# Optimization experiments

Measured on AMD Instinct MI355X. Metric: run time of the kernel, lower is better.

The kernel has to match this reference:

```python
import jax, jax.numpy as jnp
import numpy as np
import math


def _alibi_slopes(h):
    # h must be a power of 2 here (h=16); matches pow2slopes in the source
    start = 2.0 ** (-2.0 ** (-(math.log2(h) - 3.0)))
    return jnp.asarray([start ** (i + 1) for i in range(h)], dtype=jnp.float32)


def setup_inputs() -> dict:
    key = jax.random.key(0)
    ks = jax.random.split(key, 7)
    B, N, d, h, r = 2, 2048, 1024, 16, 32
    dk = d // h
    x = jax.random.normal(ks[0], (B, N, d), dtype=jnp.float32)
    # causal additive mask (standard usage of the optional `mask` arg)
    i = jnp.arange(N)[:, None]
    j = jnp.arange(N)[None, :]
    mask = jnp.where(j > i, jnp.float32(-1e9), jnp.float32(0.0))[None, None]  # [1,1,N,N]
    s = 1.0 / math.sqrt(d)
    Wq = jax.random.normal(ks[1], (d, d), dtype=jnp.float32) * s
    Wk = jax.random.normal(ks[2], (d, d), dtype=jnp.float32) * s
    Wv = jax.random.normal(ks[3], (d, d), dtype=jnp.float32) * s
    # orthogonal init of U, as in nn.init.orthogonal_
    U, _ = jnp.linalg.qr(jax.random.normal(ks[4], (dk, r), dtype=jnp.float32))
    Wproj = jax.random.normal(ks[5], (d, h * r), dtype=jnp.float32) * (1.0 / math.sqrt(h * r))
    return {"x": x, "mask": mask, "Wq": Wq, "Wk": Wk, "Wv": Wv, "U": U,
            "Wproj": Wproj, "rel_bias_tokens": N}


def reference(x, mask, Wq, Wk, Wv, U, Wproj, rel_bias_tokens):
    B, N, d = x.shape
    dk, r = U.shape
    h = d // dk

    def lowrank_proj(W):
        # Linear(d,d,bias=False) then per-head low-rank projection by U
        y = (x @ W.T).reshape(B, N, h, dk)          # [B,N,h,dk]
        return jnp.einsum('bnhk,kr->bhnr', y, U)     # [B,h,N,r]

    q = lowrank_proj(Wq)
    k = lowrank_proj(Wk)
    v = lowrank_proj(Wv)

    # scores scaled by sqrt(dk) (NOT sqrt(r)) -- faithful to source
    att = jnp.einsum('bhnr,bhmr->bhnm', q, k) / math.sqrt(dk)  # [B,h,N,N]

    # q_len == k_len branch: alibi bias + mask
    i = jnp.arange(rel_bias_tokens)[:, None]
    j = jnp.arange(rel_bias_tokens)[None, :]
    dist = jnp.maximum(j - i, 0).astype(att.dtype)             # clamp_min(0)
    slopes = _alibi_slopes(h)
    att = att + (-slopes[:, None, None] * dist)[None] + mask

    z = jnp.einsum('bhnm,bhmr->bhnr', jax.nn.softmax(att, axis=-1), v)
    z = z.transpose(0, 2, 1, 3).reshape(B, N, h * r)
    # dropout is identity in eval
    return z @ Wproj.T
```

## Files before the change

kernel.cpp:

```cpp
#include <hip/hip_runtime.h>
#include <hip/hip_bf16.h>
#include <stdint.h>

typedef unsigned short u16;
typedef __attribute__((ext_vector_type(4))) short short4v;
typedef __attribute__((ext_vector_type(8))) short short8;
typedef __attribute__((ext_vector_type(4))) float f32x4;

#define NB 2
#define NN 2048
#define ND 1024
#define NH 16
#define NR 32
#define NM (NB*NN)
#define NHR 512
#define NQKV 1536

static __device__ __forceinline__ u16 f2bf(float f) {
  union { float f; uint32_t u; } v; v.f = f;
  uint32_t r = v.u + 0x7fffu + ((v.u >> 16) & 1u);
  return (u16)(r >> 16);
}
static __device__ __forceinline__ u16 fastbf(float f) {
  union { float f; uint32_t u; } v; v.f = f;
  return (u16)((v.u + 0x8000u) >> 16);
}

typedef __attribute__((address_space(1))) unsigned int as1_u32;
typedef __attribute__((address_space(3))) unsigned int as3_u32;

static __device__ __forceinline__ void async_copy16(void* lds, const void* g) {
  __builtin_amdgcn_global_load_lds((as1_u32*)(uintptr_t)g,
                                   (as3_u32*)(uint32_t)(uintptr_t)lds,
                                   16, 0, 0);
}

#define SB_BARRIER() do {                                        \
    asm volatile("s_waitcnt vmcnt(0) lgkmcnt(0)" ::: "memory");  \
    __syncthreads();                                             \
  } while (0)

__global__ __launch_bounds__(256, 2)
void prep(const float* __restrict__ x, const float* __restrict__ Wproj,
          const float* __restrict__ Wq, const float* __restrict__ Wk,
          const float* __restrict__ Wv, const float* __restrict__ U,
          u16* __restrict__ xb, u16* __restrict__ Wpb, u16* __restrict__ WcT) {
  __shared__ float sU[64 * 32];
  const int blk = blockIdx.x;
  const int tid = threadIdx.x;
  if (blk < 2304) {
    const float* in = (blk < 2048) ? x : Wproj;
    u16* o = (blk < 2048) ? xb : Wpb;
    const int i = ((blk < 2048) ? blk : (blk - 2048)) * 256 + tid;
    const float4* p = (const float4*)in + (size_t)i * 2;
    float4 a = p[0], b2 = p[1];
    short8 v;
    v[0] = f2bf(a.x);  v[1] = f2bf(a.y);  v[2] = f2bf(a.z);  v[3] = f2bf(a.w);
    v[4] = f2bf(b2.x); v[5] = f2bf(b2.y); v[6] = f2bf(b2.z); v[7] = f2bf(b2.w);
    *((short8*)o + i) = v;
  } else {
    #pragma unroll
    for (int t = 0; t < 2; ++t)
      ((float4*)sU)[t * 256 + tid] = ((const float4*)U)[t * 256 + tid];
    __syncthreads();
    const int local = blk - 2304;
    const int wh = local >> 2;
    const int w = wh >> 4, head = wh & 15;
    const float* W = (w == 0) ? Wq : (w == 1 ? Wk : Wv);
    const int i = (local & 3) * 256 + tid;
    const float* Wcol = W + (size_t)head * 64 * ND + i;
    float acc[32];
    #pragma unroll
    for (int rr = 0; rr < 32; ++rr) acc[rr] = 0.f;
    for (int kk = 0; kk < 64; ++kk) {
      const float wv = Wcol[(size_t)kk * ND];
      const float4* u4 = (const float4*)&sU[kk * 32];
      #pragma unroll
      for (int r4 = 0; r4 < 8; ++r4) {
        float4 u = u4[r4];
        acc[r4 * 4 + 0] += wv * u.x;
        acc[r4 * 4 + 1] += wv * u.y;
        acc[r4 * 4 + 2] += wv * u.z;
        acc[r4 * 4 + 3] += wv * u.w;
      }
    }
    const float sc = (w == 0) ? 0.125f : 1.0f;
    const int colBase = w * 512 + head * 32;
    #pragma unroll
    for (int rr = 0; rr < 32; ++rr)
      WcT[(size_t)(colBase + rr) * ND + i] = f2bf(acc[rr] * sc);
  }
}

template<int EPI>
__global__ __launch_bounds__(256, 3)
void gemm_bt(const u16* __restrict__ A, int lda,
             const u16* __restrict__ BT, int ldb, int K,
             u16* __restrict__ o0, u16* __restrict__ o1, u16* __restrict__ o2,
             float* __restrict__ fo) {
  __shared__ __align__(16) u16 lA[2][64 * 64];
  __shared__ __align__(16) u16 lB[2][128 * 64];
  const int tid = threadIdx.x;
  const int lane = tid & 63, quad = lane >> 4, l16 = lane & 15;
  const int wave = tid >> 6;
  const int wn = wave * 32;
  const int GX = gridDim.x;
  const int flat = blockIdx.y * GX + blockIdx.x;
  const int xcd = flat & 7, s = flat >> 3;
  const int per = gridDim.y >> 3;
  const int brow = xcd * per + s / GX, bcol = s % GX;
  const int rowBase = brow * 64, colBase = bcol * 128;

  f32x4 acc[4][2];
  #pragma unroll
  for (int i = 0; i < 4; ++i)
    #pragma unroll
    for (int j = 0; j < 2; ++j)
      acc[i][j] = (f32x4){0.f, 0.f, 0.f, 0.f};

  #define GSTAGE(t_, bf_) do {                                              \
    const int kt0 = (t_) * 64;                                              \
    _Pragma("unroll")                                                       \
    for (int it = 0; it < 6; ++it) {                                        \
      const int cid = it * 256 + tid;                                       \
      if (it < 2) {                                                         \
        const int row = cid >> 3, pc = cid & 7;                             \
        const int gc = pc ^ (row & 7);                                      \
        async_copy16(&lA[bf_][cid * 8],                                     \
                     &A[(size_t)(rowBase + row) * lda + kt0 + gc * 8]);     \
      } else {                                                              \
        const int c2 = cid - 512;                                           \
        const int row = c2 >> 3, pc = c2 & 7;                               \
        const int gc = pc ^ (row & 7);                                      \
        async_copy16(&lB[bf_][c2 * 8],                                      \
                     &BT[(size_t)(colBase + row) * ldb + kt0 + gc * 8]);    \
      }                                                                     \
    }                                                                       \
  } while (0)

  const int NT = K / 64;
  GSTAGE(0, 0);
  int buf = 0;
  for (int t = 0; t < NT; ++t) {
    SB_BARRIER();
    if (t + 1 < NT) GSTAGE(t + 1, buf ^ 1);
    #pragma unroll
    for (int ks = 0; ks < 64; ks += 32) {
      short8 fa[4], fb[2];
      #pragma unroll
      for (int t2 = 0; t2 < 4; ++t2) {
        const int ra = t2 * 16 + l16;
        const int pa = ((ks >> 3) + quad) ^ (ra & 7);
        fa[t2] = *(const short8*)&lA[buf][ra * 64 + pa * 8];
      }
      #pragma unroll
      for (int t2 = 0; t2 < 2; ++t2) {
        const int rb = wn + t2 * 16 + l16;
        const int pb = ((ks >> 3) + quad) ^ (rb & 7);
        fb[t2] = *(const short8*)&lB[buf][rb * 64 + pb * 8];
      }
      #pragma unroll
      for (int mt = 0; mt < 4; ++mt)
        #pragma unroll
        for (int nt = 0; nt < 2; ++nt)
          acc[mt][nt] = __builtin_amdgcn_mfma_f32_16x16x32_bf16(
              fa[mt], fb[nt], acc[mt][nt], 0, 0, 0);
    }
    buf ^= 1;
  }
  #undef GSTAGE

  #pragma unroll
  for (int mt = 0; mt < 4; ++mt) {
    const int gr0 = rowBase + mt * 16 + quad * 4;
    #pragma unroll
    for (int nt = 0; nt < 2; ++nt) {
      const int c = colBase + wn + nt * 16 + l16;
      #pragma unroll
      for (int j = 0; j < 4; ++j) {
        const float v = acc[mt][nt][j];
        const int row = gr0 + j;
        if (EPI == 0) {
          fo[(size_t)row * 1024 + c] = v;
        } else {
          const int b = row >> 11, n = row & (NN - 1);
          const int w = c >> 9, ch = c & 511, head = ch >> 5, rr = ch & 31;
          if (w == 0)
            o0[(size_t)(((b * NH + head) * NN + n)) * NR + rr] = f2bf(v);
          else if (w == 1)
            o1[(size_t)(((b * NH + head) * NN + n)) * NR + rr] = f2bf(v);
          else
            o2[(size_t)((b * NH + head) * NR + rr) * NN + n] = f2bf(v);
        }
      }
    }
  }
}

__global__ __launch_bounds__(256, 6)
void flash_attn(const u16* __restrict__ q, const u16* __restrict__ k,
                const u16* __restrict__ vt, u16* __restrict__ z) {
  __shared__ __align__(16) u16 lK[2][64 * 32];
  __shared__ __align__(16) u16 lV[2][32 * 64];
  const int bh = blockIdx.x;
  const int b = bh >> 4, head = bh & 15;
  const int tid = threadIdx.x;
  const int lane = tid & 63, quad = lane >> 4, l16 = lane & 15;
  const int wave = tid >> 6;
  const int qblk = gridDim.y - 1 - blockIdx.y;
  const int qb0 = qblk * 64;
  const int qbase = qb0 + wave * 16;
  const int qq = qbase + l16;

  const u16* qp = q  + (size_t)bh * NN * NR;
  const u16* kp = k  + (size_t)bh * NN * NR;
  const u16* vp = vt + (size_t)bh * NR * NN;

  const short8 bq = *(const short8*)&qp[(size_t)(qbase + l16) * NR + quad * 8];

  f32x4 Ot0 = (f32x4){0.f,0.f,0.f,0.f};
  f32x4 Ot1 = (f32x4){0.f,0.f,0.f,0.f};
  float ls = 0.f;

  const int krow = tid >> 2, kc = tid & 3;
  const int vrow = tid >> 3, vpc = tid & 7;
  const int vgc = vpc ^ (vrow & 7);

  #define STAGE(kt_, buf_) do {                                            \
    const int m0_ = (kt_) * 64;                                            \
    async_copy16(&lK[buf_][tid * 8], &kp[(size_t)(m0_ + krow) * NR + kc * 8]); \
    async_copy16(&lV[buf_][tid * 8], &vp[(size_t)vrow * NN + m0_ + vgc * 8]);  \
  } while (0)

  STAGE(0, 0);
  int buf = 0;
  for (int kt = 0; kt <= qblk; ++kt) {
    SB_BARRIER();
    if (kt < qblk) STAGE(kt + 1, buf ^ 1);

    const int m0 = kt * 64;
    f32x4 s[4];
    const f32x4 zero = (f32x4){0.f,0.f,0.f,0.f};
    #pragma unroll
    for (int g = 0; g < 4; ++g) {
      const short8 ak = *(const short8*)&lK[buf][(16 * g + l16) * 32 + quad * 8];
      s[g] = __builtin_amdgcn_mfma_f32_16x16x32_bf16(ak, bq, zero, 0, 0, 0);
    }
    if (kt == qblk) {
      #pragma unroll
      for (int g = 0; g < 4; ++g)
        #pragma unroll
        for (int j = 0; j < 4; ++j)
          if (m0 + 16 * g + quad * 4 + j > qq) s[g][j] = -1e30f;
    }
    #pragma unroll
    for (int g = 0; g < 4; ++g) {
      const float p0 = __expf(s[g][0]), p1 = __expf(s[g][1]);
      const float p2 = __expf(s[g][2]), p3 = __expf(s[g][3]);
      ls += (p0 + p1) + (p2 + p3);
      short4v bp;
      bp[0] = fastbf(p0); bp[1] = fastbf(p1); bp[2] = fastbf(p2); bp[3] = fastbf(p3);
      const int c0 = 2 * g + (quad >> 1), off = (quad & 1) * 4;
      const short4v av0 = *(const short4v*)
          &lV[buf][l16 * 64 + ((c0 ^ (l16 & 7)) * 8) + off];
      const short4v av1 = *(const short4v*)
          &lV[buf][(16 + l16) * 64 + ((c0 ^ ((16 + l16) & 7)) * 8) + off];
      Ot0 = __builtin_amdgcn_mfma_f32_16x16x16bf16_1k(av0, bp, Ot0, 0, 0, 0);
      Ot1 = __builtin_amdgcn_mfma_f32_16x16x16bf16_1k(av1, bp, Ot1, 0, 0, 0);
    }
    buf ^= 1;
  }
  #undef STAGE

  ls += __shfl_xor(ls, 16);
  ls += __shfl_xor(ls, 32);
  const float inv = 1.f / ls;

  short4v o0, o1;
  #pragma unroll
  for (int j = 0; j < 4; ++j) {
    o0[j] = f2bf(Ot0[j] * inv);
    o1[j] = f2bf(Ot1[j] * inv);
  }
  u16* zr = z + (size_t)(b * NN + qq) * NHR + head * NR;
  *(short4v*)&zr[quad * 4]      = o0;
  *(short4v*)&zr[16 + quad * 4] = o1;
}

extern "C" void kernel_launch(void* const* d_in, const int* in_sizes, int n_in,
                              void* d_out, int out_size, void* d_ws, size_t ws_size,
                              hipStream_t stream) {
  const float* x     = (const float*)d_in[0];
  const float* Wq    = (const float*)d_in[2];
  const float* Wk    = (const float*)d_in[3];
  const float* Wv    = (const float*)d_in[4];
  const float* U     = (const float*)d_in[5];
  const float* Wproj = (const float*)d_in[6];
  float* out = (float*)d_out;

  u16* ws  = (u16*)d_ws;
  u16* xb  = ws;
  u16* z   = ws;
  u16* Wpb = ws + (size_t)4 * 1024 * 1024;
  u16* WcT = Wpb + (size_t)512 * 1024;
  u16* q   = ws + (size_t)6 * 1024 * 1024;
  u16* kk  = q  + (size_t)NB * NH * NN * NR;
  u16* vt  = kk + (size_t)NB * NH * NN * NR;

  prep<<<2496, 256, 0, stream>>>(x, Wproj, Wq, Wk, Wv, U, xb, Wpb, WcT);
  gemm_bt<1><<<dim3(NQKV / 128, NM / 64), 256, 0, stream>>>(
      xb, ND, WcT, ND, ND, q, kk, vt, nullptr);
  flash_attn<<<dim3(NB * NH, NN / 64), 256, 0, stream>>>(q, kk, vt, z);
  gemm_bt<0><<<dim3(ND / 128, NM / 64), 256, 0, stream>>>(
      z, NHR, Wpb, NHR, NHR, nullptr, nullptr, nullptr, out);
}
```

Before: 160.4 us.

## Process 128 query rows per attention block, reuse K/V tiles, use exp2

The flash attention kernel now handles 128 query rows per block, with each wave owning two 16-row fragments. Each staged K/V tile therefore feeds twice as many MFMAs, halving K/V staging and barriers per query. The grid pairs long and short causal blocks by interleaving qblk order, and the log2e factor is folded into the Q weight scale so the kernel can use the native exp2. The costs are higher register pressure, occupancy lowered to 2 in launch bounds, and half as many blocks in flight.

Result: slower. 165.5 us (+3.2%).

```diff
diff --git a/kernel.cpp b/kernel.cpp
--- a/kernel.cpp
+++ b/kernel.cpp
@@ -25,6 +25,12 @@
   union { float f; uint32_t u; } v; v.f = f;
   return (u16)((v.u + 0x8000u) >> 16);
 }
+
+#if __has_builtin(__builtin_amdgcn_exp2f)
+#define EXP2(x) __builtin_amdgcn_exp2f(x)
+#else
+#define EXP2(x) exp2f(x)
+#endif
 
 typedef __attribute__((address_space(1))) unsigned int as1_u32;
 typedef __attribute__((address_space(3))) unsigned int as3_u32;
@@ -84,7 +90,7 @@
         acc[r4 * 4 + 3] += wv * u.w;
       }
     }
-    const float sc = (w == 0) ? 0.125f : 1.0f;
+    const float sc = (w == 0) ? 0.125f * 1.44269504088896340736f : 1.0f;
     const int colBase = w * 512 + head * 32;
     #pragma unroll
     for (int rr = 0; rr < 32; ++rr)
@@ -197,7 +203,7 @@
   }
 }
 
-__global__ __launch_bounds__(256, 6)
+__global__ __launch_bounds__(256, 2)
 void flash_attn(const u16* __restrict__ q, const u16* __restrict__ k,
                 const u16* __restrict__ vt, u16* __restrict__ z) {
   __shared__ __align__(16) u16 lK[2][64 * 32];
@@ -207,20 +213,26 @@
   const int tid = threadIdx.x;
   const int lane = tid & 63, quad = lane >> 4, l16 = lane & 15;
   const int wave = tid >> 6;
-  const int qblk = gridDim.y - 1 - blockIdx.y;
-  const int qb0 = qblk * 64;
-  const int qbase = qb0 + wave * 16;
-  const int qq = qbase + l16;
+  const int y = blockIdx.y;
+  const int half = gridDim.y >> 1;
+  const int qblk = (y < half) ? (gridDim.y - 1 - y) : (y - half);
+  const int qb0 = qblk * 128;
+  const int qbase = qb0 + wave * 32;
 
   const u16* qp = q  + (size_t)bh * NN * NR;
   const u16* kp = k  + (size_t)bh * NN * NR;
   const u16* vp = vt + (size_t)bh * NR * NN;
 
-  const short8 bq = *(const short8*)&qp[(size_t)(qbase + l16) * NR + quad * 8];
-
-  f32x4 Ot0 = (f32x4){0.f,0.f,0.f,0.f};
-  f32x4 Ot1 = (f32x4){0.f,0.f,0.f,0.f};
-  float ls = 0.f;
+  const short8 bq0 = *(const short8*)&qp[(size_t)(qbase + l16) * NR + quad * 8];
+  const short8 bq1 = *(const short8*)&qp[(size_t)(qbase + 16 + l16) * NR + quad * 8];
+
+  f32x4 Ot[2][2];
+  #pragma unroll
+  for (int qf = 0; qf < 2; ++qf)
+    #pragma unroll
+    for (int hh = 0; hh < 2; ++hh)
+      Ot[qf][hh] = (f32x4){0.f, 0.f, 0.f, 0.f};
+  float lsum[2] = {0.f, 0.f};
 
   const int krow = tid >> 2, kc = tid & 3;
   const int vrow = tid >> 3, vpc = tid & 7;
@@ -234,57 +246,71 @@
 
   STAGE(0, 0);
   int buf = 0;
-  for (int kt = 0; kt <= qblk; ++kt) {
+  const int NT = 2 * qblk + 2;
+  for (int kt = 0; kt < NT; ++kt) {
     SB_BARRIER();
-    if (kt < qblk) STAGE(kt + 1, buf ^ 1);
+    if (kt + 1 < NT) STAGE(kt + 1, buf ^ 1);
 
     const int m0 = kt * 64;
-    f32x4 s[4];
-    const f32x4 zero = (f32x4){0.f,0.f,0.f,0.f};
+    f32x4 s[2][4];
+    const f32x4 zero = (f32x4){0.f, 0.f, 0.f, 0.f};
     #pragma unroll
     for (int g = 0; g < 4; ++g) {
       const short8 ak = *(const short8*)&lK[buf][(16 * g + l16) * 32 + quad * 8];
-      s[g] = __builtin_amdgcn_mfma_f32_16x16x32_bf16(ak, bq, zero, 0, 0, 0);
-    }
-    if (kt == qblk) {
-      #pragma unroll
-      for (int g = 0; g < 4; ++g)
+      s[0][g] = __builtin_amdgcn_mfma_f32_16x16x32_bf16(ak, bq0, zero, 0, 0, 0);
+      s[1][g] = __builtin_amdgcn_mfma_f32_16x16x32_bf16(ak, bq1, zero, 0, 0, 0);
+    }
+    #pragma unroll
+    for (int qf = 0; qf < 2; ++qf) {
+      const int qrow0 = qbase + qf * 16;
+      if (m0 + 63 > qrow0) {
+        const int qqf = qrow0 + l16;
         #pragma unroll
-        for (int j = 0; j < 4; ++j)
-          if (m0 + 16 * g + quad * 4 + j > qq) s[g][j] = -1e30f;
+        for (int g = 0; g < 4; ++g)
+          #pragma unroll
+          for (int j = 0; j < 4; ++j)
+            if (m0 + 16 * g + quad * 4 + j > qqf) s[qf][g][j] = -1e30f;
+      }
     }
     #pragma unroll
     for (int g = 0; g < 4; ++g) {
-      const float p0 = __expf(s[g][0]), p1 = __expf(s[g][1]);
-      const float p2 = __expf(s[g][2]), p3 = __expf(s[g][3]);
-      ls += (p0 + p1) + (p2 + p3);
-      short4v bp;
-      bp[0] = fastbf(p0); bp[1] = fastbf(p1); bp[2] = fastbf(p2); bp[3] = fastbf(p3);
       const int c0 = 2 * g + (quad >> 1), off = (quad & 1) * 4;
       const short4v av0 = *(const short4v*)
           &lV[buf][l16 * 64 + ((c0 ^ (l16 & 7)) * 8) + off];
       const short4v av1 = *(const short4v*)
           &lV[buf][(16 + l16) * 64 + ((c0 ^ ((16 + l16) & 7)) * 8) + off];
-      Ot0 = __builtin_amdgcn_mfma_f32_16x16x16bf16_1k(av0, bp, Ot0, 0, 0, 0);
-      Ot1 = __builtin_amdgcn_mfma_f32_16x16x16bf16_1k(av1, bp, Ot1, 0, 0, 0);
+      #pragma unroll
+      for (int qf = 0; qf < 2; ++qf) {
+        const float p0 = EXP2(s[qf][g][0]), p1 = EXP2(s[qf][g][1]);
+        const float p2 = EXP2(s[qf][g][2]), p3 = EXP2(s[qf][g][3]);
+        lsum[qf] += (p0 + p1) + (p2 + p3);
+        short4v bp;
+        bp[0] = fastbf(p0); bp[1] = fastbf(p1);
+        bp[2] = fastbf(p2); bp[3] = fastbf(p3);
+        Ot[qf][0] = __builtin_amdgcn_mfma_f32_16x16x16bf16_1k(av0, bp, Ot[qf][0], 0, 0, 0);
+        Ot[qf][1] = __builtin_amdgcn_mfma_f32_16x16x16bf16_1k(av1, bp, Ot[qf][1], 0, 0, 0);
+      }
     }
     buf ^= 1;
   }
   #undef STAGE
 
-  ls += __shfl_xor(ls, 16);
-  ls += __shfl_xor(ls, 32);
-  const float inv = 1.f / ls;
-
-  short4v o0, o1;
   #pragma unroll
-  for (int j = 0; j < 4; ++j) {
-    o0[j] = f2bf(Ot0[j] * inv);
-    o1[j] = f2bf(Ot1[j] * inv);
-  }
-  u16* zr = z + (size_t)(b * NN + qq) * NHR + head * NR;
-  *(short4v*)&zr[quad * 4]      = o0;
-  *(short4v*)&zr[16 + quad * 4] = o1;
+  for (int qf = 0; qf < 2; ++qf) {
+    float ls = lsum[qf];
+    ls += __shfl_xor(ls, 16);
+    ls += __shfl_xor(ls, 32);
+    const float inv = 1.f / ls;
+    short4v o0, o1;
+    #pragma unroll
+    for (int j = 0; j < 4; ++j) {
+      o0[j] = f2bf(Ot[qf][0][j] * inv);
+      o1[j] = f2bf(Ot[qf][1][j] * inv);
+    }
+    u16* zr = z + (size_t)(b * NN + qbase + qf * 16 + l16) * NHR + head * NR;
+    *(short4v*)&zr[quad * 4]      = o0;
+    *(short4v*)&zr[16 + quad * 4] = o1;
+  }
 }
 
 extern "C" void kernel_launch(void* const* d_in, const int* in_sizes, int n_in,
@@ -310,7 +336,7 @@
   prep<<<2496, 256, 0, stream>>>(x, Wproj, Wq, Wk, Wv, U, xb, Wpb, WcT);
   gemm_bt<1><<<dim3(NQKV / 128, NM / 64), 256, 0, stream>>>(
       xb, ND, WcT, ND, ND, q, kk, vt, nullptr);
-  flash_attn<<<dim3(NB * NH, NN / 64), 256, 0, stream>>>(q, kk, vt, z);
+  flash_attn<<<dim3(NB * NH, NN / 128), 256, 0, stream>>>(q, kk, vt, z);
   gemm_bt<0><<<dim3(ND / 128, NM / 64), 256, 0, stream>>>(
       z, NHR, Wpb, NHR, NHR, nullptr, nullptr, nullptr, out);
 }
```

## Fuse x fp32-to-bf16 conversion into QKV GEMM load and use exp2 softmax

Applied to the files above, without the earlier changes.

Drops the separate pass that converted x to bf16 in workspace. The QKV GEMM now loads fp32 A tiles into registers, converts them, and writes them to LDS after the MFMA step, overlapping with compute. The Q scale folds in log2(e) so the attention softmax can use a native exp2 instead of __expf. This removes a full write and read of x at the cost of more register use and synchronous global loads in the GEMM.

Measured after the change: 161.7 us. About the same (+0.8%).

```diff
diff --git a/kernel.cpp b/kernel.cpp
--- a/kernel.cpp
+++ b/kernel.cpp
@@ -26,6 +26,12 @@
   return (u16)((v.u + 0x8000u) >> 16);
 }
 
+#if __has_builtin(__builtin_amdgcn_exp2f)
+#define EXP2(x) __builtin_amdgcn_exp2f(x)
+#else
+#define EXP2(x) __builtin_exp2f(x)
+#endif
+
 typedef __attribute__((address_space(1))) unsigned int as1_u32;
 typedef __attribute__((address_space(3))) unsigned int as3_u32;
 
@@ -41,29 +47,27 @@
   } while (0)
 
 __global__ __launch_bounds__(256, 2)
-void prep(const float* __restrict__ x, const float* __restrict__ Wproj,
+void prep(const float* __restrict__ Wproj,
           const float* __restrict__ Wq, const float* __restrict__ Wk,
           const float* __restrict__ Wv, const float* __restrict__ U,
-          u16* __restrict__ xb, u16* __restrict__ Wpb, u16* __restrict__ WcT) {
+          u16* __restrict__ Wpb, u16* __restrict__ WcT) {
   __shared__ float sU[64 * 32];
   const int blk = blockIdx.x;
   const int tid = threadIdx.x;
-  if (blk < 2304) {
-    const float* in = (blk < 2048) ? x : Wproj;
-    u16* o = (blk < 2048) ? xb : Wpb;
-    const int i = ((blk < 2048) ? blk : (blk - 2048)) * 256 + tid;
-    const float4* p = (const float4*)in + (size_t)i * 2;
+  if (blk < 256) {
+    const int i = blk * 256 + tid;
+    const float4* p = (const float4*)Wproj + (size_t)i * 2;
     float4 a = p[0], b2 = p[1];
     short8 v;
     v[0] = f2bf(a.x);  v[1] = f2bf(a.y);  v[2] = f2bf(a.z);  v[3] = f2bf(a.w);
     v[4] = f2bf(b2.x); v[5] = f2bf(b2.y); v[6] = f2bf(b2.z); v[7] = f2bf(b2.w);
-    *((short8*)o + i) = v;
+    *((short8*)Wpb + i) = v;
   } else {
     #pragma unroll
     for (int t = 0; t < 2; ++t)
       ((float4*)sU)[t * 256 + tid] = ((const float4*)U)[t * 256 + tid];
     __syncthreads();
-    const int local = blk - 2304;
+    const int local = blk - 256;
     const int wh = local >> 2;
     const int w = wh >> 4, head = wh & 15;
     const float* W = (w == 0) ? Wq : (w == 1 ? Wk : Wv);
@@ -84,7 +88,7 @@
         acc[r4 * 4 + 3] += wv * u.w;
       }
     }
-    const float sc = (w == 0) ? 0.125f : 1.0f;
+    const float sc = (w == 0) ? 0.125f * 1.44269504088896340736f : 1.0f;
     const int colBase = w * 512 + head * 32;
     #pragma unroll
     for (int rr = 0; rr < 32; ++rr)
@@ -92,14 +96,16 @@
   }
 }
 
-template<int EPI>
+template<int EPI, int LF32>
 __global__ __launch_bounds__(256, 3)
-void gemm_bt(const u16* __restrict__ A, int lda,
+void gemm_bt(const void* __restrict__ Av, int lda,
              const u16* __restrict__ BT, int ldb, int K,
              u16* __restrict__ o0, u16* __restrict__ o1, u16* __restrict__ o2,
              float* __restrict__ fo) {
   __shared__ __align__(16) u16 lA[2][64 * 64];
   __shared__ __align__(16) u16 lB[2][128 * 64];
+  const u16* Ab = (const u16*)Av;
+  const float* Af = (const float*)Av;
   const int tid = threadIdx.x;
   const int lane = tid & 63, quad = lane >> 4, l16 = lane & 15;
   const int wave = tid >> 6;
@@ -118,32 +124,68 @@
     for (int j = 0; j < 2; ++j)
       acc[i][j] = (f32x4){0.f, 0.f, 0.f, 0.f};
 
-  #define GSTAGE(t_, bf_) do {                                              \
+  #define GSTAGE_B(t_, bf_) do {                                            \
     const int kt0 = (t_) * 64;                                              \
     _Pragma("unroll")                                                       \
-    for (int it = 0; it < 6; ++it) {                                        \
+    for (int it = 0; it < 4; ++it) {                                        \
+      const int c2 = it * 256 + tid;                                        \
+      const int row = c2 >> 3, pc = c2 & 7;                                 \
+      const int gc = pc ^ (row & 7);                                        \
+      async_copy16(&lB[bf_][c2 * 8],                                        \
+                   &BT[(size_t)(colBase + row) * ldb + kt0 + gc * 8]);      \
+    }                                                                       \
+  } while (0)
+
+  #define GSTAGE_A16(t_, bf_) do {                                          \
+    const int kt0 = (t_) * 64;                                              \
+    _Pragma("unroll")                                                       \
+    for (int it = 0; it < 2; ++it) {                                        \
       const int cid = it * 256 + tid;                                       \
-      if (it < 2) {                                                         \
-        const int row = cid >> 3, pc = cid & 7;                             \
-        const int gc = pc ^ (row & 7);                                      \
-        async_copy16(&lA[bf_][cid * 8],                                     \
-                     &A[(size_t)(rowBase + row) * lda + kt0 + gc * 8]);     \
-      } else {                                                              \
-        const int c2 = cid - 512;                                           \
-        const int row = c2 >> 3, pc = c2 & 7;                               \
-        const int gc = pc ^ (row & 7);                                      \
-        async_copy16(&lB[bf_][c2 * 8],                                      \
-                     &BT[(size_t)(colBase + row) * ldb + kt0 + gc * 8]);    \
-      }                                                                     \
+      const int row = cid >> 3, pc = cid & 7;                               \
+      const int gc = pc ^ (row & 7);                                        \
+      async_copy16(&lA[bf_][cid * 8],                                       \
+                   &Ab[(size_t)(rowBase + row) * lda + kt0 + gc * 8]);      \
     }                                                                       \
   } while (0)
 
+  float4 areg[4];
+  #define ALOAD(t_) do {                                                    \
+    const int kt0 = (t_) * 64;                                              \
+    _Pragma("unroll")                                                       \
+    for (int it = 0; it < 2; ++it) {                                        \
+      const int cid = it * 256 + tid;                                       \
+      const int row = cid >> 3, pc = cid & 7;                               \
+      const int gc = pc ^ (row & 7);                                        \
+      const float4* src = (const float4*)                                   \
+          &Af[(size_t)(rowBase + row) * lda + kt0 + gc * 8];                \
+      areg[it * 2 + 0] = src[0];                                            \
+      areg[it * 2 + 1] = src[1];                                            \
+    }                                                                       \
+  } while (0)
+  #define AWRITE(bf_) do {                                                  \
+    _Pragma("unroll")                                                       \
+    for (int it = 0; it < 2; ++it) {                                        \
+      const int cid = it * 256 + tid;                                       \
+      const float4 a = areg[it * 2 + 0], b2 = areg[it * 2 + 1];             \
+      short8 v8;                                                            \
+      v8[0] = f2bf(a.x);  v8[1] = f2bf(a.y);                                \
+      v8[2] = f2bf(a.z);  v8[3] = f2bf(a.w);                                \
+      v8[4] = f2bf(b2.x); v8[5] = f2bf(b2.y);                               \
+      v8[6] = f2bf(b2.z); v8[7] = f2bf(b2.w);                               \
+      *(short8*)&lA[bf_][cid * 8] = v8;                                     \
+    }                                                                       \
+  } while (0)
+
   const int NT = K / 64;
-  GSTAGE(0, 0);
+  if (LF32) { ALOAD(0); GSTAGE_B(0, 0); AWRITE(0); }
+  else      { GSTAGE_A16(0, 0); GSTAGE_B(0, 0); }
   int buf = 0;
   for (int t = 0; t < NT; ++t) {
     SB_BARRIER();
-    if (t + 1 < NT) GSTAGE(t + 1, buf ^ 1);
+    if (t + 1 < NT) {
+      if (LF32) { ALOAD(t + 1); GSTAGE_B(t + 1, buf ^ 1); }
+      else      { GSTAGE_A16(t + 1, buf ^ 1); GSTAGE_B(t + 1, buf ^ 1); }
+    }
     #pragma unroll
     for (int ks = 0; ks < 64; ks += 32) {
       short8 fa[4], fb[2];
@@ -166,9 +208,13 @@
           acc[mt][nt] = __builtin_amdgcn_mfma_f32_16x16x32_bf16(
               fa[mt], fb[nt], acc[mt][nt], 0, 0, 0);
     }
+    if (LF32 && t + 1 < NT) AWRITE(buf ^ 1);
     buf ^= 1;
   }
-  #undef GSTAGE
+  #undef GSTAGE_B
+  #undef GSTAGE_A16
+  #undef ALOAD
+  #undef AWRITE
 
   #pragma unroll
   for (int mt = 0; mt < 4; ++mt) {
@@ -255,8 +301,8 @@
     }
     #pragma unroll
     for (int g = 0; g < 4; ++g) {
-      const float p0 = __expf(s[g][0]), p1 = __expf(s[g][1]);
-      const float p2 = __expf(s[g][2]), p3 = __expf(s[g][3]);
+      const float p0 = EXP2(s[g][0]), p1 = EXP2(s[g][1]);
+      const float p2 = EXP2(s[g][2]), p3 = EXP2(s[g][3]);
       ls += (p0 + p1) + (p2 + p3);
       short4v bp;
       bp[0] = fastbf(p0); bp[1] = fastbf(p1); bp[2] = fastbf(p2); bp[3] = fastbf(p3);
@@ -299,7 +345,6 @@
   float* out = (float*)d_out;
 
   u16* ws  = (u16*)d_ws;
-  u16* xb  = ws;
   u16* z   = ws;
   u16* Wpb = ws + (size_t)4 * 1024 * 1024;
   u16* WcT = Wpb + (size_t)512 * 1024;
@@ -307,10 +352,10 @@
   u16* kk  = q  + (size_t)NB * NH * NN * NR;
   u16* vt  = kk + (size_t)NB * NH * NN * NR;
 
-  prep<<<2496, 256, 0, stream>>>(x, Wproj, Wq, Wk, Wv, U, xb, Wpb, WcT);
-  gemm_bt<1><<<dim3(NQKV / 128, NM / 64), 256, 0, stream>>>(
-      xb, ND, WcT, ND, ND, q, kk, vt, nullptr);
+  prep<<<448, 256, 0, stream>>>(Wproj, Wq, Wk, Wv, U, Wpb, WcT);
+  gemm_bt<1, 1><<<dim3(NQKV / 128, NM / 64), 256, 0, stream>>>(
+      x, ND, WcT, ND, ND, q, kk, vt, nullptr);
   flash_attn<<<dim3(NB * NH, NN / 64), 256, 0, stream>>>(q, kk, vt, z);
-  gemm_bt<0><<<dim3(ND / 128, NM / 64), 256, 0, stream>>>(
+  gemm_bt<0, 0><<<dim3(ND / 128, NM / 64), 256, 0, stream>>>(
       z, NHR, Wpb, NHR, NHR, nullptr, nullptr, nullptr, out);
 }
```

## Stage V-transpose epilogue through LDS and fold log2e into Q for exp2

Applied to the files above, without the earlier changes.

In the QKV GEMM epilogue, blocks producing V columns now write bf16 results into LDS transposed, then emit 16-byte coalesced stores to the transposed V layout. This replaces strided 2-byte scattered stores. Separately, the log2(e) factor is folded into the Q weight scale so the attention softmax can use the native exp2 instruction instead of __expf. This reuses the GEMM's LDS buffer after an extra barrier, and slightly changes bf16 rounding of Q.

Measured after the change: 157.4 us. No clear change (-1.8%).

```diff
diff --git a/kernel.cpp b/kernel.cpp
--- a/kernel.cpp
+++ b/kernel.cpp
@@ -25,6 +25,12 @@
   union { float f; uint32_t u; } v; v.f = f;
   return (u16)((v.u + 0x8000u) >> 16);
 }
+
+#if __has_builtin(__builtin_amdgcn_exp2f)
+#define EXP2(x) __builtin_amdgcn_exp2f(x)
+#else
+#define EXP2(x) __builtin_exp2f(x)
+#endif
 
 typedef __attribute__((address_space(1))) unsigned int as1_u32;
 typedef __attribute__((address_space(3))) unsigned int as3_u32;
@@ -84,7 +90,7 @@
         acc[r4 * 4 + 3] += wv * u.w;
       }
     }
-    const float sc = (w == 0) ? 0.125f : 1.0f;
+    const float sc = (w == 0) ? 0.125f * 1.44269504088896340736f : 1.0f;
     const int colBase = w * 512 + head * 32;
     #pragma unroll
     for (int rr = 0; rr < 32; ++rr)
@@ -98,8 +104,9 @@
              const u16* __restrict__ BT, int ldb, int K,
              u16* __restrict__ o0, u16* __restrict__ o1, u16* __restrict__ o2,
              float* __restrict__ fo) {
-  __shared__ __align__(16) u16 lA[2][64 * 64];
-  __shared__ __align__(16) u16 lB[2][128 * 64];
+  __shared__ __align__(16) u16 lds[2 * 64 * 64 + 2 * 128 * 64];
+  #define LA(bf) (&lds[(bf) * (64 * 64)])
+  #define LB(bf) (&lds[2 * 64 * 64 + (bf) * (128 * 64)])
   const int tid = threadIdx.x;
   const int lane = tid & 63, quad = lane >> 4, l16 = lane & 15;
   const int wave = tid >> 6;
@@ -126,13 +133,13 @@
       if (it < 2) {                                                         \
         const int row = cid >> 3, pc = cid & 7;                             \
         const int gc = pc ^ (row & 7);                                      \
-        async_copy16(&lA[bf_][cid * 8],                                     \
+        async_copy16(&LA(bf_)[cid * 8],                                     \
                      &A[(size_t)(rowBase + row) * lda + kt0 + gc * 8]);     \
       } else {                                                              \
         const int c2 = cid - 512;                                           \
         const int row = c2 >> 3, pc = c2 & 7;                               \
         const int gc = pc ^ (row & 7);                                      \
-        async_copy16(&lB[bf_][c2 * 8],                                      \
+        async_copy16(&LB(bf_)[c2 * 8],                                      \
                      &BT[(size_t)(colBase + row) * ldb + kt0 + gc * 8]);    \
       }                                                                     \
     }                                                                       \
@@ -151,13 +158,13 @@
       for (int t2 = 0; t2 < 4; ++t2) {
         const int ra = t2 * 16 + l16;
         const int pa = ((ks >> 3) + quad) ^ (ra & 7);
-        fa[t2] = *(const short8*)&lA[buf][ra * 64 + pa * 8];
+        fa[t2] = *(const short8*)&LA(buf)[ra * 64 + pa * 8];
       }
       #pragma unroll
       for (int t2 = 0; t2 < 2; ++t2) {
         const int rb = wn + t2 * 16 + l16;
         const int pb = ((ks >> 3) + quad) ^ (rb & 7);
-        fb[t2] = *(const short8*)&lB[buf][rb * 64 + pb * 8];
+        fb[t2] = *(const short8*)&LB(buf)[rb * 64 + pb * 8];
       }
       #pragma unroll
       for (int mt = 0; mt < 4; ++mt)
@@ -169,6 +176,36 @@
     buf ^= 1;
   }
   #undef GSTAGE
+
+  if (EPI == 1 && colBase >= 1024) {
+    __syncthreads();
+    u16* ldsT = &lds[0];
+    const int ST = 72;
+    #pragma unroll
+    for (int nt = 0; nt < 2; ++nt) {
+      const int lc = wn + nt * 16 + l16;
+      #pragma unroll
+      for (int mt = 0; mt < 4; ++mt) {
+        short4v t4;
+        #pragma unroll
+        for (int j = 0; j < 4; ++j) t4[j] = f2bf(acc[mt][nt][j]);
+        *(short4v*)&ldsT[lc * ST + mt * 16 + quad * 4] = t4;
+      }
+    }
+    __syncthreads();
+    const int b = rowBase >> 11;
+    #pragma unroll
+    for (int it = 0; it < 4; ++it) {
+      const int chunk = it * 256 + tid;
+      const int lc = chunk >> 3, part = chunk & 7;
+      const short8 vv = *(const short8*)&ldsT[lc * ST + part * 8];
+      const int c = colBase + lc;
+      const int head = (c >> 5) & 15, rr = c & 31;
+      const int n0 = (rowBase & (NN - 1)) + part * 8;
+      *(short8*)&o2[((size_t)((b * NH + head) * NR + rr)) * NN + n0] = vv;
+    }
+    return;
+  }
 
   #pragma unroll
   for (int mt = 0; mt < 4; ++mt) {
@@ -187,14 +224,14 @@
           const int w = c >> 9, ch = c & 511, head = ch >> 5, rr = ch & 31;
           if (w == 0)
             o0[(size_t)(((b * NH + head) * NN + n)) * NR + rr] = f2bf(v);
-          else if (w == 1)
+          else
             o1[(size_t)(((b * NH + head) * NN + n)) * NR + rr] = f2bf(v);
-          else
-            o2[(size_t)((b * NH + head) * NR + rr) * NN + n] = f2bf(v);
         }
       }
     }
   }
+  #undef LA
+  #undef LB
 }
 
 __global__ __launch_bounds__(256, 6)
@@ -255,8 +292,8 @@
     }
     #pragma unroll
     for (int g = 0; g < 4; ++g) {
-      const float p0 = __expf(s[g][0]), p1 = __expf(s[g][1]);
-      const float p2 = __expf(s[g][2]), p3 = __expf(s[g][3]);
+      const float p0 = EXP2(s[g][0]), p1 = EXP2(s[g][1]);
+      const float p2 = EXP2(s[g][2]), p3 = EXP2(s[g][3]);
       ls += (p0 + p1) + (p2 + p3);
       short4v bp;
       bp[0] = fastbf(p0); bp[1] = fastbf(p1); bp[2] = fastbf(p2); bp[3] = fastbf(p3);
```
